# Optimization experiments

Hardware: AMD Instinct MI355X
Metric: run time of the kernel (lower is better)

The kernel has to match this reference:

```python
import jax, jax.numpy as jnp
import numpy as np

B, C, H, W = 32, 1, 512, 512
NUM_SPIXEL = 100
W_RGB, W_FREQ = 0.5, 0.5


def setup_inputs() -> dict:
    key = jax.random.key(0)
    k1, k2, k3, k4 = jax.random.split(key, 4)
    out_map_rgb = jax.random.uniform(k1, (B, C, H, W), dtype=jnp.float32)
    out_map_freq = jax.random.uniform(k2, (B, C, H, W), dtype=jnp.float32)
    label = jax.random.randint(k3, (B,), 0, 2, dtype=jnp.int32)
    spixel = jax.random.randint(k4, (B, C, H, W), 0, NUM_SPIXEL, dtype=jnp.int32)
    return {"out_map_rgb": out_map_rgb, "out_map_freq": out_map_freq,
            "label": label, "spixel": spixel}


def _spixel_mean_map(weighted_sum, spixel, num_spixel):
    # Segment-mean over superpixels, vectorized across the batch by offsetting
    # each image's ids into a disjoint segment range [b*num_spixel, (b+1)*num_spixel).
    b = weighted_sum.shape[0]
    ids = spixel.reshape(b, -1) + (jnp.arange(b, dtype=spixel.dtype)[:, None] * num_spixel)
    ids = ids.reshape(-1)                      # [B*C*H*W]
    vals = weighted_sum.reshape(-1)            # [B*C*H*W]
    nseg = b * num_spixel
    sums = jax.ops.segment_sum(vals, ids, num_segments=nseg)
    counts = jax.ops.segment_sum(jnp.ones_like(vals), ids, num_segments=nseg)
    means = sums / jnp.maximum(counts, 1.0)    # empty segments -> 0 (never gathered)
    return means[ids].reshape(weighted_sum.shape)


def reference(out_map_rgb, out_map_freq, label, spixel):
    # weighted multi-view sum (computed under no_grad in the original)
    tgt_map = W_RGB * out_map_rgb + W_FREQ * out_map_freq
    # per-superpixel mean (the hot segment-reduce)
    tgt_map = _spixel_mean_map(tgt_map, spixel, NUM_SPIXEL)
    # soft=True: no thresholding. zeros_on_au: zero target where label == 0
    is_pos = (label != 0)[:, None, None, None]
    tgt_map = jnp.where(is_pos, tgt_map, 0.0)
    tgt_map = jax.lax.stop_gradient(tgt_map)   # requires_grad=False / no_grad
    loss_rgb = jnp.mean((out_map_rgb - tgt_map) ** 2)
    loss_freq = jnp.mean((out_map_freq - tgt_map) ** 2)
    total_loss = loss_rgb + loss_freq
    return total_loss, tgt_map
```

## Files before the change

kernel.cpp:

```cpp
#include <hip/hip_runtime.h>

#define B_     32
#define HW_    (512 * 512)
#define NSP    100
#define NSEG   (B_ * NSP)
#define NTOT   ((double)(B_ * (size_t)HW_))
#define CHUNKS 64

#define REP      16
#define RSTRIDE  101
#define FIXS   256.f
#define FIXINV (1.f / 256.f)
#define SUMMASK ((1ull << 44) - 1)

__global__ void mvc_init(unsigned long long* seg) {
    int i = blockIdx.x * blockDim.x + threadIdx.x;
    if (i < NSEG) seg[i] = 0ull;
}

__global__ void mvc_segsum(const float* __restrict__ rgb,
                           const float* __restrict__ freq,
                           const int*   __restrict__ spx,
                           unsigned long long* __restrict__ seg,
                           float* __restrict__ partials) {
    __shared__ unsigned bins[REP * RSTRIDE];
    const int b = blockIdx.y;
    for (int i = threadIdx.x; i < REP * RSTRIDE; i += blockDim.x) bins[i] = 0u;
    __syncthreads();

    const int base = (threadIdx.x & (REP - 1)) * RSTRIDE;

    const float4* r4 = (const float4*)(rgb + (size_t)b * HW_);
    const float4* f4 = (const float4*)(freq + (size_t)b * HW_);
    const int4*   s4 = (const int4*)(spx + (size_t)b * HW_);
    const int n4 = HW_ / 4;
    float sq = 0.f;
    for (int i = blockIdx.x * blockDim.x + threadIdx.x; i < n4;
         i += gridDim.x * blockDim.x) {
        float4 rv = r4[i];
        float4 fv = f4[i];
        int4   sv = s4[i];
        sq += rv.x * rv.x + fv.x * fv.x;
        sq += rv.y * rv.y + fv.y * fv.y;
        sq += rv.z * rv.z + fv.z * fv.z;
        sq += rv.w * rv.w + fv.w * fv.w;
        unsigned fx0 = (unsigned)((rv.x + fv.x) * 128.f + 0.5f);
        unsigned fx1 = (unsigned)((rv.y + fv.y) * 128.f + 0.5f);
        unsigned fx2 = (unsigned)((rv.z + fv.z) * 128.f + 0.5f);
        unsigned fx3 = (unsigned)((rv.w + fv.w) * 128.f + 0.5f);
        atomicAdd(&bins[base + sv.x], (1u << 20) | fx0);
        atomicAdd(&bins[base + sv.y], (1u << 20) | fx1);
        atomicAdd(&bins[base + sv.z], (1u << 20) | fx2);
        atomicAdd(&bins[base + sv.w], (1u << 20) | fx3);
    }
    __syncthreads();

    for (int i = threadIdx.x; i < NSP; i += blockDim.x) {
        unsigned long long c = 0, s = 0;
        #pragma unroll
        for (int r = 0; r < REP; ++r) {
            unsigned v = bins[r * RSTRIDE + i];
            c += v >> 20;
            s += v & 0xFFFFFu;
        }
        if (c) atomicAdd(&seg[b * NSP + i], (c << 44) | s);
    }

    for (int off = 32; off > 0; off >>= 1) sq += __shfl_down(sq, off, 64);
    __shared__ float wsf[4];
    const int wid = threadIdx.x >> 6;
    if ((threadIdx.x & 63) == 0) wsf[wid] = sq;
    __syncthreads();
    if (threadIdx.x == 0)
        partials[blockIdx.y * CHUNKS + blockIdx.x] =
            wsf[0] + wsf[1] + wsf[2] + wsf[3];
}

__global__ void mvc_finalize(const int*   __restrict__ spx,
                             const int*   __restrict__ label,
                             const unsigned long long* __restrict__ seg,
                             const float* __restrict__ partials,
                             float* __restrict__ out) {
    __shared__ float lm[NSP];
    const int b = blockIdx.y;
    const float pos = (label[b] != 0) ? 1.f : 0.f;
    for (int i = threadIdx.x; i < NSP; i += blockDim.x) {
        unsigned long long v = seg[b * NSP + i];
        float n = (float)(v >> 44);
        float S = (float)(v & SUMMASK) * FIXINV;
        lm[i] = pos * S / fmaxf(n, 1.f);
    }
    __syncthreads();

    const int4* s4 = (const int4*)(spx + (size_t)b * HW_);
    float4* t4 = (float4*)(out + 1 + (size_t)b * HW_);
    const int n4 = HW_ / 4;
    for (int i = blockIdx.x * blockDim.x + threadIdx.x; i < n4;
         i += gridDim.x * blockDim.x) {
        int4 sv = s4[i];
        t4[i] = make_float4(lm[sv.x], lm[sv.y], lm[sv.z], lm[sv.w]);
    }

    if (blockIdx.x == 0 && blockIdx.y == 0) {
        double corr = 0.0;
        for (int i = threadIdx.x; i < NSEG; i += blockDim.x) {
            unsigned long long v = seg[i];
            float n = (float)(v >> 44);
            float S = (float)(v & SUMMASK) * FIXINV;
            int bb = i / NSP;
            float t = (label[bb] != 0) ? (S / fmaxf(n, 1.f)) : 0.f;
            corr += -4.0 * (double)t * (double)S
                    + 2.0 * (double)n * (double)t * (double)t;
        }
        for (int i = threadIdx.x; i < CHUNKS * B_; i += blockDim.x)
            corr += (double)partials[i];
        for (int off = 32; off > 0; off >>= 1) corr += __shfl_down(corr, off, 64);
        __shared__ double wsd[4];
        const int wid = threadIdx.x >> 6;
        if ((threadIdx.x & 63) == 0) wsd[wid] = corr;
        __syncthreads();
        if (threadIdx.x == 0)
            out[0] = (float)((wsd[0] + wsd[1] + wsd[2] + wsd[3]) / NTOT);
    }
}

extern "C" void kernel_launch(void* const* d_in, const int* in_sizes, int n_in,
                              void* d_out, int out_size, void* d_ws, size_t ws_size,
                              hipStream_t stream) {
    const float* rgb   = (const float*)d_in[0];
    const float* freq  = (const float*)d_in[1];
    const int*   label = (const int*)d_in[2];
    const int*   spx   = (const int*)d_in[3];
    float* out = (float*)d_out;

    unsigned long long* seg = (unsigned long long*)d_ws;
    float* partials = (float*)(seg + NSEG);

    mvc_init<<<(NSEG + 255) / 256, 256, 0, stream>>>(seg);

    dim3 grid(CHUNKS, B_);
    mvc_segsum<<<grid, 256, 0, stream>>>(rgb, freq, spx, seg, partials);

    mvc_finalize<<<grid, 256, 0, stream>>>(spx, label, seg, partials, out);
}
```

Baseline: 41.03 us.

## Replace global atomics with per-block partials and distribute final loss reduction

Each segsum block now writes its per-superpixel packed count/sum to a private partials slot instead of doing global atomics, which removes the zero-init kernel. The finalize kernel reduces the 64 chunk partials per image in shared memory, uses 32 chunks with a fixed unrolled loop for the gather-write, and computes per-image correction terms in parallel rather than in a single serial block. A small third kernel produces the final scalar loss. The cost is extra partials traffic and an extra launch, and the correction accumulation moves from double to float precision.

```diff
diff --git a/kernel.cpp b/kernel.cpp
--- a/kernel.cpp
+++ b/kernel.cpp
@@ -1,42 +1,41 @@
 #include <hip/hip_runtime.h>
 
-#define B_     32
-#define HW_    (512 * 512)
-#define NSP    100
-#define NSEG   (B_ * NSP)
-#define NTOT   ((double)(B_ * (size_t)HW_))
-#define CHUNKS 64
+#define B_      32
+#define HW_     (512 * 512)
+#define NSP     100
+#define NTOT    ((double)(B_ * (size_t)HW_))
+
+#define CHUNKS1 64
+#define NBLK1   (CHUNKS1 * B_)
+#define CHUNKS2 32
+#define F4PB2   (HW_ / 4 / CHUNKS2)
+#define ITERS2  (F4PB2 / 256)
 
 #define REP      16
 #define RSTRIDE  101
-#define FIXS   256.f
-#define FIXINV (1.f / 256.f)
+#define FIXINV  (1.f / 256.f)
 #define SUMMASK ((1ull << 44) - 1)
-
-__global__ void mvc_init(unsigned long long* seg) {
-    int i = blockIdx.x * blockDim.x + threadIdx.x;
-    if (i < NSEG) seg[i] = 0ull;
-}
 
 __global__ void mvc_segsum(const float* __restrict__ rgb,
                            const float* __restrict__ freq,
                            const int*   __restrict__ spx,
-                           unsigned long long* __restrict__ seg,
-                           float* __restrict__ partials) {
+                           unsigned long long* __restrict__ partials,
+                           float* __restrict__ sqp) {
     __shared__ unsigned bins[REP * RSTRIDE];
+    const int tid = threadIdx.x;
     const int b = blockIdx.y;
-    for (int i = threadIdx.x; i < REP * RSTRIDE; i += blockDim.x) bins[i] = 0u;
+    const int bid = b * CHUNKS1 + blockIdx.x;
+    for (int i = tid; i < REP * RSTRIDE; i += 256) bins[i] = 0u;
     __syncthreads();
 
-    const int base = (threadIdx.x & (REP - 1)) * RSTRIDE;
+    const int base = (tid & (REP - 1)) * RSTRIDE;
 
     const float4* r4 = (const float4*)(rgb + (size_t)b * HW_);
     const float4* f4 = (const float4*)(freq + (size_t)b * HW_);
     const int4*   s4 = (const int4*)(spx + (size_t)b * HW_);
     const int n4 = HW_ / 4;
     float sq = 0.f;
-    for (int i = blockIdx.x * blockDim.x + threadIdx.x; i < n4;
-         i += gridDim.x * blockDim.x) {
+    for (int i = blockIdx.x * 256 + tid; i < n4; i += CHUNKS1 * 256) {
         float4 rv = r4[i];
         float4 fv = f4[i];
         int4   sv = s4[i];
@@ -55,72 +54,86 @@
     }
     __syncthreads();
 
-    for (int i = threadIdx.x; i < NSP; i += blockDim.x) {
-        unsigned long long c = 0, s = 0;
+    for (int i = tid; i < NSP; i += 256) {
+        unsigned long long cc = 0, ss = 0;
         #pragma unroll
         for (int r = 0; r < REP; ++r) {
             unsigned v = bins[r * RSTRIDE + i];
-            c += v >> 20;
-            s += v & 0xFFFFFu;
+            cc += v >> 20;
+            ss += v & 0xFFFFFu;
         }
-        if (c) atomicAdd(&seg[b * NSP + i], (c << 44) | s);
+        partials[(size_t)bid * NSP + i] = (cc << 44) | ss;
     }
 
     for (int off = 32; off > 0; off >>= 1) sq += __shfl_down(sq, off, 64);
     __shared__ float wsf[4];
-    const int wid = threadIdx.x >> 6;
-    if ((threadIdx.x & 63) == 0) wsf[wid] = sq;
+    if ((tid & 63) == 0) wsf[tid >> 6] = sq;
     __syncthreads();
-    if (threadIdx.x == 0)
-        partials[blockIdx.y * CHUNKS + blockIdx.x] =
-            wsf[0] + wsf[1] + wsf[2] + wsf[3];
+    if (tid == 0) sqp[bid] = wsf[0] + wsf[1] + wsf[2] + wsf[3];
 }
 
 __global__ void mvc_finalize(const int*   __restrict__ spx,
                              const int*   __restrict__ label,
-                             const unsigned long long* __restrict__ seg,
-                             const float* __restrict__ partials,
+                             const unsigned long long* __restrict__ partials,
+                             float* __restrict__ corrs,
                              float* __restrict__ out) {
+    __shared__ unsigned long long ps[2 * NSP];
     __shared__ float lm[NSP];
-    const int b = blockIdx.y;
+    __shared__ float cr[NSP];
+    const int tid = threadIdx.x;
+    const int c = blockIdx.x, b = blockIdx.y;
     const float pos = (label[b] != 0) ? 1.f : 0.f;
-    for (int i = threadIdx.x; i < NSP; i += blockDim.x) {
-        unsigned long long v = seg[b * NSP + i];
+
+    if (tid < 2 * NSP) {
+        const int bin = tid % NSP, half = tid / NSP;
+        const unsigned long long* pb =
+            partials + ((size_t)b * CHUNKS1 + half * (CHUNKS1 / 2)) * NSP + bin;
+        unsigned long long acc = 0;
+        #pragma unroll 4
+        for (int k = 0; k < CHUNKS1 / 2; ++k) acc += pb[(size_t)k * NSP];
+        ps[tid] = acc;
+    }
+    __syncthreads();
+    if (tid < NSP) {
+        unsigned long long v = ps[tid] + ps[tid + NSP];
         float n = (float)(v >> 44);
         float S = (float)(v & SUMMASK) * FIXINV;
-        lm[i] = pos * S / fmaxf(n, 1.f);
+        float t = pos * S / fmaxf(n, 1.f);
+        lm[tid] = t;
+        cr[tid] = -4.f * t * S + 2.f * n * t * t;
     }
     __syncthreads();
 
-    const int4* s4 = (const int4*)(spx + (size_t)b * HW_);
-    float4* t4 = (float4*)(out + 1 + (size_t)b * HW_);
-    const int n4 = HW_ / 4;
-    for (int i = blockIdx.x * blockDim.x + threadIdx.x; i < n4;
-         i += gridDim.x * blockDim.x) {
-        int4 sv = s4[i];
-        t4[i] = make_float4(lm[sv.x], lm[sv.y], lm[sv.z], lm[sv.w]);
+    const int4* s4 = (const int4*)spx + (size_t)b * (HW_/4) + (size_t)c * F4PB2;
+    float4* t4 = (float4*)(out + 1) + (size_t)b * (HW_/4) + (size_t)c * F4PB2;
+    #pragma unroll
+    for (int k = 0; k < ITERS2; ++k) {
+        const int idx = k * 256 + tid;
+        int4 sv = s4[idx];
+        t4[idx] = make_float4(lm[sv.x], lm[sv.y], lm[sv.z], lm[sv.w]);
     }
 
-    if (blockIdx.x == 0 && blockIdx.y == 0) {
-        double corr = 0.0;
-        for (int i = threadIdx.x; i < NSEG; i += blockDim.x) {
-            unsigned long long v = seg[i];
-            float n = (float)(v >> 44);
-            float S = (float)(v & SUMMASK) * FIXINV;
-            int bb = i / NSP;
-            float t = (label[bb] != 0) ? (S / fmaxf(n, 1.f)) : 0.f;
-            corr += -4.0 * (double)t * (double)S
-                    + 2.0 * (double)n * (double)t * (double)t;
-        }
-        for (int i = threadIdx.x; i < CHUNKS * B_; i += blockDim.x)
-            corr += (double)partials[i];
-        for (int off = 32; off > 0; off >>= 1) corr += __shfl_down(corr, off, 64);
-        __shared__ double wsd[4];
-        const int wid = threadIdx.x >> 6;
-        if ((threadIdx.x & 63) == 0) wsd[wid] = corr;
-        __syncthreads();
-        if (threadIdx.x == 0)
-            out[0] = (float)((wsd[0] + wsd[1] + wsd[2] + wsd[3]) / NTOT);
+    if (c == 0 && tid == 0) {
+        float s = 0.f;
+        for (int i = 0; i < NSP; ++i) s += cr[i];
+        corrs[b] = s;
+    }
+}
+
+__global__ void mvc_loss(const float* __restrict__ sqp,
+                         const float* __restrict__ corrs,
+                         float* __restrict__ out) {
+    const int tid = threadIdx.x;
+    double s = 0.0;
+    for (int i = tid; i < NBLK1; i += 256) s += (double)sqp[i];
+    for (int off = 32; off > 0; off >>= 1) s += __shfl_down(s, off, 64);
+    __shared__ double wsd[4];
+    if ((tid & 63) == 0) wsd[tid >> 6] = s;
+    __syncthreads();
+    if (tid == 0) {
+        double tot = wsd[0] + wsd[1] + wsd[2] + wsd[3];
+        for (int i = 0; i < B_; ++i) tot += (double)corrs[i];
+        out[0] = (float)(tot / NTOT);
     }
 }
 
@@ -133,13 +146,13 @@
     const int*   spx   = (const int*)d_in[3];
     float* out = (float*)d_out;
 
-    unsigned long long* seg = (unsigned long long*)d_ws;
-    float* partials = (float*)(seg + NSEG);
+    unsigned long long* partials = (unsigned long long*)d_ws;
+    float* sqp   = (float*)(partials + (size_t)NBLK1 * NSP);
+    float* corrs = sqp + NBLK1;
 
-    mvc_init<<<(NSEG + 255) / 256, 256, 0, stream>>>(seg);
-
-    dim3 grid(CHUNKS, B_);
-    mvc_segsum<<<grid, 256, 0, stream>>>(rgb, freq, spx, seg, partials);
-
-    mvc_finalize<<<grid, 256, 0, stream>>>(spx, label, seg, partials, out);
+    mvc_segsum<<<dim3(CHUNKS1, B_), 256, 0, stream>>>(rgb, freq, spx,
+                                                      partials, sqp);
+    mvc_finalize<<<dim3(CHUNKS2, B_), 256, 0, stream>>>(spx, label, partials,
+                                                        corrs, out);
+    mvc_loss<<<1, 256, 0, stream>>>(sqp, corrs, out);
 }
```

Result: faster. 37.85 us (-7.8%).
